# Kernel tuning notes

Hardware: AMD Instinct MI355X
Metric: run time of the kernel (lower is better)

Reference implementation:

```python
import jax, jax.numpy as jnp
import numpy as np

M, T, D, H = 2, 2048, 1024, 16
HD = D // H
SCALE = 1.0 / np.sqrt(D).astype(np.float32)  # original divides by sqrt(emb_dim)


def setup_inputs() -> dict:
    key = jax.random.key(0)
    ks = jax.random.split(key, 8)
    def lin(k):
        kw, kb = jax.random.split(k)
        W = jax.random.normal(kw, (D, D), dtype=jnp.float32) * (1.0 / np.sqrt(D))
        b = jax.random.normal(kb, (D,), dtype=jnp.float32) * 0.01
        return W, b
    Wq, bq = lin(ks[0]); Wk, bk = lin(ks[1]); Wv, bv = lin(ks[2]); Wo, bo = lin(ks[3])
    Q = jax.random.normal(ks[4], (M, T, D), dtype=jnp.float32)
    K = jax.random.normal(ks[5], (M, T, D), dtype=jnp.float32)
    V = jax.random.normal(ks[6], (M, T, D), dtype=jnp.float32)
    mask = jnp.ones((M, 1, 1, T), dtype=jnp.int32)
    return {"Q": Q, "K": K, "V": V, "mask": mask,
            "Wq": Wq, "bq": bq, "Wk": Wk, "bk": bk,
            "Wv": Wv, "bv": bv, "Wo": Wo, "bo": bo}


def reference(Q, K, V, mask, Wq, bq, Wk, bk, Wv, bv, Wo, bo):
    m = Q.shape[0]
    # torch nn.Linear: y = x @ W.T + b
    q = (Q @ Wq.T + bq).reshape(m, -1, H, HD)  # (m, Tq, h, hd)
    k = (K @ Wk.T + bk).reshape(m, -1, H, HD)
    v = (V @ Wv.T + bv).reshape(m, -1, H, HD)
    energy = jnp.einsum('mqhd,mkhd->mhqk', q, k) * SCALE
    if mask is not None:
        energy = jnp.where(mask == 0, jnp.float32(-1e20), energy)
    attn = jax.nn.softmax(energy, axis=3)  # dropout is identity at inference
    out = jnp.einsum('mhqk,mkhd->mqhd', attn, v)  # (m, Tq, h, hd)
    concat = out.reshape(m, -1, H * HD)
    return concat @ Wo.T + bo
```

## Files before the change

kernel.cpp:

```cpp
#include <hip/hip_runtime.h>
#include <cstdint>
#include <cstddef>

#define T_SEQ 2048
#define D_EMB 1024
#define H_HEADS 16
#define MROWS 4096
#define SC2 (0.03125f * 1.44269504f)
#define MASKNEG (-1e30f)

typedef __attribute__((ext_vector_type(8))) short bf16x8;
typedef __attribute__((ext_vector_type(4))) float f32x4;
typedef __attribute__((ext_vector_type(4))) unsigned short us4;

__device__ __forceinline__ unsigned short f2bf(float f) {
  union { float f; uint32_t u; } v; v.f = f;
  uint32_t u = v.u;
  return (unsigned short)((u + 0x7FFFu + ((u >> 16) & 1u)) >> 16);
}

__device__ __forceinline__ uint32_t cvtpk(float lo, float hi) {
  uint32_t r;
  asm("v_cvt_pk_bf16_f32 %0, %1, %2" : "=v"(r) : "v"(lo), "v"(hi));
  return r;
}

__device__ __forceinline__ float fexp2(float x) {
  float r;
  asm("v_exp_f32 %0, %1" : "=v"(r) : "v"(x));
  return r;
}

__device__ __forceinline__ void gl16(const void* g, void* l) {
  __builtin_amdgcn_global_load_lds(
      (const __attribute__((address_space(1))) unsigned int*)g,
      (__attribute__((address_space(3))) unsigned int*)l, 16, 0, 0);
}

__global__ __launch_bounds__(256) void cvt_all(
    const float* __restrict__ Q, const float* __restrict__ K, const float* __restrict__ V,
    const float* __restrict__ Wq, const float* __restrict__ Wk,
    const float* __restrict__ Wv, const float* __restrict__ Wo,
    unsigned short* __restrict__ Qb, unsigned short* __restrict__ Kb,
    unsigned short* __restrict__ Vb,
    unsigned short* __restrict__ Wqb, unsigned short* __restrict__ Wkb,
    unsigned short* __restrict__ Wvb, unsigned short* __restrict__ Wob) {
  int i = blockIdx.x * 256 + threadIdx.x;
  const float* src;
  unsigned short* dst;
  int j;
  if (i < 3145728) {
    int s = i >> 20;
    j = i & 1048575;
    src = (s == 0) ? Q : (s == 1) ? K : V;
    dst = (s == 0) ? Qb : (s == 1) ? Kb : Vb;
  } else {
    int k = i - 3145728;
    int s = k >> 18;
    j = k & 262143;
    src = (s == 0) ? Wq : (s == 1) ? Wk : (s == 2) ? Wv : Wo;
    dst = (s == 0) ? Wqb : (s == 1) ? Wkb : (s == 2) ? Wvb : Wob;
  }
  float4 f = ((const float4*)src)[j];
  us4 o;
  o[0] = f2bf(f.x); o[1] = f2bf(f.y); o[2] = f2bf(f.z); o[3] = f2bf(f.w);
  ((us4*)dst)[j] = o;
}

__global__ __launch_bounds__(256) void qkv_gemm(
    const unsigned short* __restrict__ Qb, const unsigned short* __restrict__ Kb,
    const unsigned short* __restrict__ Vb,
    const unsigned short* __restrict__ Wqb, const unsigned short* __restrict__ Wkb,
    const unsigned short* __restrict__ Wvb,
    const float* __restrict__ bq, const float* __restrict__ bk, const float* __restrict__ bv,
    unsigned short* __restrict__ qo, unsigned short* __restrict__ ko,
    unsigned short* __restrict__ vto) {
  const int swz = (blockIdx.x & 7) * 96 + (blockIdx.x >> 3);
  const int bx = swz & 7, by = (swz >> 3) & 31, z = swz >> 8;
  const unsigned short* A = (z == 0) ? Qb : (z == 1) ? Kb : Vb;
  const unsigned short* W = (z == 0) ? Wqb : (z == 1) ? Wkb : Wvb;
  const float* bias = (z == 0) ? bq : (z == 1) ? bk : bv;

  __shared__ __align__(16) unsigned short Asm[2][128 * 32];
  __shared__ __align__(16) unsigned short Bsm[2][128 * 32];

  const int tid = threadIdx.x;
  const int lane = tid & 63, w = tid >> 6;
  const int fq = lane >> 4, fr = lane & 15;
  const int brow = by * 128, bcol = bx * 128;
  const int wr = (w >> 1) * 64, wc = (w & 1) * 64;

  f32x4 acc[4][4] = {};

#define QKV_STAGE(buf, k0)                                                     \
  {                                                                            \
    _Pragma("unroll") for (int it = 0; it < 2; ++it) {                         \
      int idx = it * 256 + tid;                                                \
      int row = idx >> 2, ce = (idx & 3) * 8;                                  \
      gl16(&A[(size_t)(brow + row) * D_EMB + (k0) + ce],                       \
           (char*)Asm[buf] + idx * 16);                                        \
      gl16(&W[(size_t)(bcol + row) * D_EMB + (k0) + ce],                       \
           (char*)Bsm[buf] + idx * 16);                                        \
    }                                                                          \
  }

#define QKV_COMPUTE(buf)                                                       \
  {                                                                            \
    bf16x8 af[4], bfr[4];                                                      \
    _Pragma("unroll") for (int i = 0; i < 4; ++i)                              \
        af[i] = *(const bf16x8*)((const char*)Asm[buf] +                       \
                                 (wr + i * 16 + fr) * 64 + fq * 16);           \
    _Pragma("unroll") for (int j = 0; j < 4; ++j)                              \
        bfr[j] = *(const bf16x8*)((const char*)Bsm[buf] +                      \
                                  (wc + j * 16 + fr) * 64 + fq * 16);          \
    _Pragma("unroll") for (int i = 0; i < 4; ++i)                              \
        _Pragma("unroll") for (int j = 0; j < 4; ++j)                          \
            acc[i][j] = __builtin_amdgcn_mfma_f32_16x16x32_bf16(               \
                af[i], bfr[j], acc[i][j], 0, 0, 0);                            \
  }

  QKV_STAGE(0, 0);
  __syncthreads();
#pragma unroll 1
  for (int t = 0; t < 32; t += 2) {
    QKV_STAGE(1, (t + 1) * 32);
    QKV_COMPUTE(0);
    __syncthreads();
    if (t + 2 < 32) QKV_STAGE(0, (t + 2) * 32);
    QKV_COMPUTE(1);
    __syncthreads();
  }

#pragma unroll
  for (int i = 0; i < 4; ++i) {
#pragma unroll
    for (int j = 0; j < 4; ++j) {
      int r0 = brow + wr + i * 16 + fq * 4;
      int cc = bcol + wc + j * 16 + fr;
      float bb = bias[cc];
      if (z < 2) {
        unsigned short* O = (z == 0) ? qo : ko;
#pragma unroll
        for (int q = 0; q < 4; ++q)
          O[(size_t)(r0 + q) * D_EMB + cc] = f2bf(acc[i][j][q] + bb);
      } else {
        int hh = cc >> 6, dd = cc & 63;
        int mm = r0 >> 11, tt = r0 & 2047;
        us4 pk;
#pragma unroll
        for (int q = 0; q < 4; ++q) pk[q] = f2bf(acc[i][j][q] + bb);
        *(us4*)&vto[((size_t)((mm * H_HEADS + hh) * 64 + dd)) * T_SEQ + tt] = pk;
      }
    }
  }
}

__global__ __launch_bounds__(256) void out_gemm(const unsigned short* __restrict__ Ab,
                                                const unsigned short* __restrict__ Wb,
                                                const float* __restrict__ bias,
                                                float* __restrict__ Out) {
  const int swz = (blockIdx.x & 7) * 64 + (blockIdx.x >> 3);
  const int bx = swz & 15, by = swz >> 4;

  __shared__ __align__(16) unsigned short Asm[2][128 * 32];
  __shared__ __align__(16) unsigned short Bsm[2][64 * 32];
  const int tid = threadIdx.x;
  const int lane = tid & 63, w = tid >> 6;
  const int fq = lane >> 4, fr = lane & 15;
  const int brow = by * 128, bcol = bx * 64;
  const int wr = w * 32;

  f32x4 acc[2][4] = {};

#define OUT_STAGE(buf, k0)                                                     \
  {                                                                            \
    _Pragma("unroll") for (int it = 0; it < 2; ++it) {                         \
      int idx = it * 256 + tid;                                                \
      int row = idx >> 2, ce = (idx & 3) * 8;                                  \
      gl16(&Ab[(size_t)(brow + row) * D_EMB + (k0) + ce],                      \
           (char*)Asm[buf] + idx * 16);                                        \
    }                                                                          \
    {                                                                          \
      int row = tid >> 2, ce = (tid & 3) * 8;                                  \
      gl16(&Wb[(size_t)(bcol + row) * D_EMB + (k0) + ce],                      \
           (char*)Bsm[buf] + tid * 16);                                        \
    }                                                                          \
  }

#define OUT_COMPUTE(buf)                                                       \
  {                                                                            \
    bf16x8 af[2], bfr[4];                                                      \
    _Pragma("unroll") for (int i = 0; i < 2; ++i)                              \
        af[i] = *(const bf16x8*)((const char*)Asm[buf] +                       \
                                 (wr + i * 16 + fr) * 64 + fq * 16);           \
    _Pragma("unroll") for (int j = 0; j < 4; ++j)                              \
        bfr[j] = *(const bf16x8*)((const char*)Bsm[buf] +                      \
                                  (j * 16 + fr) * 64 + fq * 16);               \
    _Pragma("unroll") for (int i = 0; i < 2; ++i)                              \
        _Pragma("unroll") for (int j = 0; j < 4; ++j)                          \
            acc[i][j] = __builtin_amdgcn_mfma_f32_16x16x32_bf16(               \
                af[i], bfr[j], acc[i][j], 0, 0, 0);                            \
  }

  OUT_STAGE(0, 0);
  __syncthreads();
#pragma unroll 1
  for (int t = 0; t < 32; t += 2) {
    OUT_STAGE(1, (t + 1) * 32);
    OUT_COMPUTE(0);
    __syncthreads();
    if (t + 2 < 32) OUT_STAGE(0, (t + 2) * 32);
    OUT_COMPUTE(1);
    __syncthreads();
  }

#pragma unroll
  for (int i = 0; i < 2; ++i)
#pragma unroll
    for (int j = 0; j < 4; ++j) {
      int r0 = brow + wr + i * 16 + fq * 4;
      int cc = bcol + j * 16 + fr;
      float bb = bias[cc];
#pragma unroll
      for (int q = 0; q < 4; ++q)
        Out[(size_t)(r0 + q) * D_EMB + cc] = acc[i][j][q] + bb;
    }
}

__global__ __launch_bounds__(256) void attn_fwd(const unsigned short* __restrict__ qb,
                                                const unsigned short* __restrict__ kb,
                                                const unsigned short* __restrict__ vtb,
                                                const int* __restrict__ maskg,
                                                unsigned short* __restrict__ outb) {
  const int swzb = (blockIdx.x & 7) * 128 + (blockIdx.x >> 3);
  const int qt = swzb & 31, h = (swzb >> 5) & 15, mI = swzb >> 9;
  const int tid = threadIdx.x;
  const int lane = tid & 63, w = tid >> 6;
  const int fq = lane >> 4, fr = lane & 15;
  const int x_fr = (fr & 7) << 4;

  __shared__ __align__(16) unsigned short Ksm[128 * 64];
  __shared__ __align__(16) unsigned short Vsm[64 * 128];
  __shared__ __align__(16) unsigned short Psm[4][16 * 128];
  __shared__ __align__(16) float Msm[128];

  char* KsmB = (char*)Ksm;
  char* VsmB = (char*)Vsm;
  char* PsmB = (char*)Psm + w * 4096;

  const int qrow = qt * 64 + w * 16 + fr;
  bf16x8 qf[2];
#pragma unroll
  for (int kk = 0; kk < 2; ++kk)
    qf[kk] = *(const bf16x8*)&qb[((size_t)(mI * T_SEQ) + qrow) * D_EMB + h * 64 + kk * 32 + fq * 8];

  f32x4 o[4] = {};
  float mi = -1e30f, li = 0.f;

  const unsigned short* kpan = kb + (size_t)(mI * T_SEQ) * D_EMB + h * 64;
  const unsigned short* vpan = vtb + (size_t)(mI * H_HEADS + h) * 64 * T_SEQ;

  for (int k0 = 0; k0 < T_SEQ; k0 += 128) {
#pragma unroll
    for (int it = 0; it < 4; ++it) {
      int idx = it * 256 + tid;
      int row = idx >> 3;
      int sb = ((idx & 7) * 16) ^ ((row & 7) << 4);
      gl16(kpan + (size_t)(k0 + row) * D_EMB + (sb >> 1), KsmB + idx * 16);
    }
#pragma unroll
    for (int it = 0; it < 4; ++it) {
      int idx = it * 256 + tid;
      int row = idx >> 4;
      int sb = ((idx & 15) * 16) ^ ((row & 7) << 4);
      gl16(vpan + (size_t)row * T_SEQ + k0 + (sb >> 1), VsmB + idx * 16);
    }
    if (tid < 128) Msm[tid] = (maskg[mI * T_SEQ + k0 + tid] == 0) ? MASKNEG : 0.f;
    __syncthreads();

    f32x4 s[8];
#pragma unroll
    for (int mt = 0; mt < 8; ++mt) {
      const char* kr = KsmB + (mt * 16 + fr) * 128;
      bf16x8 a0 = *(const bf16x8*)(kr + ((fq * 16) ^ x_fr));
      bf16x8 a1 = *(const bf16x8*)(kr + ((64 + fq * 16) ^ x_fr));
      f32x4 t = {};
      t = __builtin_amdgcn_mfma_f32_16x16x32_bf16(a0, qf[0], t, 0, 0, 0);
      t = __builtin_amdgcn_mfma_f32_16x16x32_bf16(a1, qf[1], t, 0, 0, 0);
      s[mt] = t;
    }

    float tmax = -3e38f;
#pragma unroll
    for (int mt = 0; mt < 8; ++mt) {
      f32x4 mk = *(const f32x4*)&Msm[mt * 16 + fq * 4];
#pragma unroll
      for (int j = 0; j < 4; ++j) {
        float sv = fmaf(s[mt][j], SC2, mk[j]);
        s[mt][j] = sv;
        tmax = fmaxf(tmax, sv);
      }
    }
    tmax = fmaxf(tmax, __shfl_xor(tmax, 16));
    tmax = fmaxf(tmax, __shfl_xor(tmax, 32));

    if (__any(tmax > mi + 8.f)) {
      float mnew = fmaxf(mi, tmax);
      float corr = fexp2(mi - mnew);
#pragma unroll
      for (int nt = 0; nt < 4; ++nt) {
        o[nt][0] *= corr; o[nt][1] *= corr; o[nt][2] *= corr; o[nt][3] *= corr;
      }
      li *= corr;
      mi = mnew;
    }

    float ts = 0.f;
#pragma unroll
    for (int mt = 0; mt < 8; ++mt)
#pragma unroll
      for (int j = 0; j < 4; ++j) {
        float p = fexp2(s[mt][j] - mi);
        s[mt][j] = p;
        ts += p;
      }
    ts += __shfl_xor(ts, 16);
    ts += __shfl_xor(ts, 32);
    li += ts;

#pragma unroll
    for (int mt = 0; mt < 8; ++mt) {
      uint2 pw;
      pw.x = cvtpk(s[mt][0], s[mt][1]);
      pw.y = cvtpk(s[mt][2], s[mt][3]);
      *(uint2*)(PsmB + fr * 256 + ((mt * 32 + fq * 8) ^ x_fr)) = pw;
    }

    bf16x8 pb[4];
#pragma unroll
    for (int kk = 0; kk < 4; ++kk)
      pb[kk] = *(const bf16x8*)(PsmB + fr * 256 + ((kk * 64 + fq * 16) ^ x_fr));
#pragma unroll
    for (int nt = 0; nt < 4; ++nt) {
      const char* vr = VsmB + (nt * 16 + fr) * 256;
#pragma unroll
      for (int kk = 0; kk < 4; ++kk) {
        bf16x8 va = *(const bf16x8*)(vr + ((kk * 64 + fq * 16) ^ x_fr));
        o[nt] = __builtin_amdgcn_mfma_f32_16x16x32_bf16(va, pb[kk], o[nt], 0, 0, 0);
      }
    }
    __syncthreads();
  }

  float inv = 1.f / li;
  size_t orow = (size_t)(mI * T_SEQ + qt * 64 + w * 16 + fr) * D_EMB + h * 64;
#pragma unroll
  for (int nt = 0; nt < 4; ++nt) {
    uint2 ow;
    ow.x = cvtpk(o[nt][0] * inv, o[nt][1] * inv);
    ow.y = cvtpk(o[nt][2] * inv, o[nt][3] * inv);
    *(uint2*)&outb[orow + nt * 16 + fq * 4] = ow;
  }
}

extern "C" void kernel_launch(void* const* d_in, const int* in_sizes, int n_in,
                              void* d_out, int out_size, void* d_ws, size_t ws_size,
                              hipStream_t stream) {
  const float* Q  = (const float*)d_in[0];
  const float* K  = (const float*)d_in[1];
  const float* V  = (const float*)d_in[2];
  const int* mask = (const int*)d_in[3];
  const float* Wq = (const float*)d_in[4];
  const float* bq = (const float*)d_in[5];
  const float* Wk = (const float*)d_in[6];
  const float* bk = (const float*)d_in[7];
  const float* Wv = (const float*)d_in[8];
  const float* bv = (const float*)d_in[9];
  const float* Wo = (const float*)d_in[10];
  const float* bo = (const float*)d_in[11];

  uint8_t* ws = (uint8_t*)d_ws;
  const size_t MB = 1u << 20;
  unsigned short* Wq_b = (unsigned short*)(ws + 0 * MB);
  unsigned short* Wk_b = (unsigned short*)(ws + 2 * MB);
  unsigned short* Wv_b = (unsigned short*)(ws + 4 * MB);
  unsigned short* Wo_b = (unsigned short*)(ws + 6 * MB);
  unsigned short* q_b  = (unsigned short*)(ws + 8 * MB);
  unsigned short* k_b  = (unsigned short*)(ws + 16 * MB);
  unsigned short* vt_b = (unsigned short*)(ws + 24 * MB);
  unsigned short* Qb   = (unsigned short*)(ws + 32 * MB);
  unsigned short* Kb   = (unsigned short*)(ws + 40 * MB);
  unsigned short* Vb   = (unsigned short*)(ws + 48 * MB);
  unsigned short* cc_b = (unsigned short*)(ws + 32 * MB);

  cvt_all<<<dim3(16384), dim3(256), 0, stream>>>(Q, K, V, Wq, Wk, Wv, Wo,
                                                 Qb, Kb, Vb, Wq_b, Wk_b, Wv_b, Wo_b);

  qkv_gemm<<<dim3(768), dim3(256), 0, stream>>>(
      Qb, Kb, Vb, Wq_b, Wk_b, Wv_b, bq, bk, bv, q_b, k_b, vt_b);

  attn_fwd<<<dim3(1024), dim3(256), 0, stream>>>(
      q_b, k_b, vt_b, mask, cc_b);

  out_gemm<<<dim3(512), dim3(256), 0, stream>>>(
      cc_b, Wo_b, bo, (float*)d_out);
}
```

Before: 149.4 us.

## Use 32x32 MFMA attention with 128-row query tiles and folded softmax scale

The attention kernel is restructured to process 128 query rows per block (32 per wave) using 32x32x16 bf16 MFMA for both QK^T and PV, halving the grid and doubling K/V reuse per shared-memory load. The softmax scale is folded into the q projection epilogue, and a per-block mask precheck skips mask loading and addition for fully-unmasked key tiles. This reduces K/V global traffic and per-element softmax work, at the cost of more registers per wave and fewer blocks for occupancy.

```diff
diff --git a/kernel.cpp b/kernel.cpp
--- a/kernel.cpp
+++ b/kernel.cpp
@@ -11,6 +11,7 @@
 
 typedef __attribute__((ext_vector_type(8))) short bf16x8;
 typedef __attribute__((ext_vector_type(4))) float f32x4;
+typedef __attribute__((ext_vector_type(16))) float f32x16;
 typedef __attribute__((ext_vector_type(4))) unsigned short us4;
 
 __device__ __forceinline__ unsigned short f2bf(float f) {
@@ -140,9 +141,10 @@
       float bb = bias[cc];
       if (z < 2) {
         unsigned short* O = (z == 0) ? qo : ko;
+        float sc = (z == 0) ? SC2 : 1.0f;
 #pragma unroll
         for (int q = 0; q < 4; ++q)
-          O[(size_t)(r0 + q) * D_EMB + cc] = f2bf(acc[i][j][q] + bb);
+          O[(size_t)(r0 + q) * D_EMB + cc] = f2bf((acc[i][j][q] + bb) * sc);
       } else {
         int hh = cc >> 6, dd = cc & 63;
         int mm = r0 >> 11, tt = r0 & 2047;
@@ -232,35 +234,52 @@
                                                 const unsigned short* __restrict__ vtb,
                                                 const int* __restrict__ maskg,
                                                 unsigned short* __restrict__ outb) {
-  const int swzb = (blockIdx.x & 7) * 128 + (blockIdx.x >> 3);
-  const int qt = swzb & 31, h = (swzb >> 5) & 15, mI = swzb >> 9;
+  const int swzb = (blockIdx.x & 7) * 64 + (blockIdx.x >> 3);
+  const int qt = swzb & 15, h = (swzb >> 4) & 15, mI = swzb >> 8;
   const int tid = threadIdx.x;
   const int lane = tid & 63, w = tid >> 6;
-  const int fq = lane >> 4, fr = lane & 15;
-  const int x_fr = (fr & 7) << 4;
+  const int lq = lane & 31, h2 = lane >> 5;
 
   __shared__ __align__(16) unsigned short Ksm[128 * 64];
   __shared__ __align__(16) unsigned short Vsm[64 * 128];
-  __shared__ __align__(16) unsigned short Psm[4][16 * 128];
+  __shared__ __align__(16) char Pw[4][2304];
   __shared__ __align__(16) float Msm[128];
+  __shared__ int moks[16];
 
   char* KsmB = (char*)Ksm;
   char* VsmB = (char*)Vsm;
-  char* PsmB = (char*)Psm + w * 4096;
-
-  const int qrow = qt * 64 + w * 16 + fr;
-  bf16x8 qf[2];
-#pragma unroll
-  for (int kk = 0; kk < 2; ++kk)
-    qf[kk] = *(const bf16x8*)&qb[((size_t)(mI * T_SEQ) + qrow) * D_EMB + h * 64 + kk * 32 + fq * 8];
-
-  f32x4 o[4] = {};
+  char* PwB = Pw[w];
+
+  if (tid < 16) moks[tid] = 1;
+  __syncthreads();
+  {
+    int bad = 0;
+    const int4* mg = (const int4*)&maskg[mI * T_SEQ + tid * 8];
+    int4 a = mg[0], b = mg[1];
+    bad |= (a.x == 0) | (a.y == 0) | (a.z == 0) | (a.w == 0);
+    bad |= (b.x == 0) | (b.y == 0) | (b.z == 0) | (b.w == 0);
+    if (bad) moks[tid >> 4] = 0;
+  }
+  __syncthreads();
+  int okbits = 0;
+#pragma unroll
+  for (int i = 0; i < 16; ++i) okbits |= (moks[i] != 0) << i;
+
+  const int qrow = qt * 128 + w * 32 + lq;
+  bf16x8 qf[4];
+#pragma unroll
+  for (int db = 0; db < 4; ++db)
+    qf[db] = *(const bf16x8*)&qb[((size_t)(mI * T_SEQ) + qrow) * D_EMB + h * 64 + db * 16 + h2 * 8];
+
+  f32x16 oacc[2] = {};
   float mi = -1e30f, li = 0.f;
 
   const unsigned short* kpan = kb + (size_t)(mI * T_SEQ) * D_EMB + h * 64;
   const unsigned short* vpan = vtb + (size_t)(mI * H_HEADS + h) * 64 * T_SEQ;
 
+#pragma unroll 1
   for (int k0 = 0; k0 < T_SEQ; k0 += 128) {
+    const int ok = (okbits >> (k0 >> 7)) & 1;
 #pragma unroll
     for (int it = 0; it < 4; ++it) {
       int idx = it * 256 + tid;
@@ -275,92 +294,91 @@
       int sb = ((idx & 15) * 16) ^ ((row & 7) << 4);
       gl16(vpan + (size_t)row * T_SEQ + k0 + (sb >> 1), VsmB + idx * 16);
     }
-    if (tid < 128) Msm[tid] = (maskg[mI * T_SEQ + k0 + tid] == 0) ? MASKNEG : 0.f;
-    __syncthreads();
-
-    f32x4 s[8];
-#pragma unroll
-    for (int mt = 0; mt < 8; ++mt) {
-      const char* kr = KsmB + (mt * 16 + fr) * 128;
-      bf16x8 a0 = *(const bf16x8*)(kr + ((fq * 16) ^ x_fr));
-      bf16x8 a1 = *(const bf16x8*)(kr + ((64 + fq * 16) ^ x_fr));
-      f32x4 t = {};
-      t = __builtin_amdgcn_mfma_f32_16x16x32_bf16(a0, qf[0], t, 0, 0, 0);
-      t = __builtin_amdgcn_mfma_f32_16x16x32_bf16(a1, qf[1], t, 0, 0, 0);
-      s[mt] = t;
-    }
-
-    float tmax = -3e38f;
-#pragma unroll
-    for (int mt = 0; mt < 8; ++mt) {
-      f32x4 mk = *(const f32x4*)&Msm[mt * 16 + fq * 4];
-#pragma unroll
-      for (int j = 0; j < 4; ++j) {
-        float sv = fmaf(s[mt][j], SC2, mk[j]);
-        s[mt][j] = sv;
-        tmax = fmaxf(tmax, sv);
-      }
-    }
-    tmax = fmaxf(tmax, __shfl_xor(tmax, 16));
-    tmax = fmaxf(tmax, __shfl_xor(tmax, 32));
-
-    if (__any(tmax > mi + 8.f)) {
-      float mnew = fmaxf(mi, tmax);
-      float corr = fexp2(mi - mnew);
-#pragma unroll
-      for (int nt = 0; nt < 4; ++nt) {
-        o[nt][0] *= corr; o[nt][1] *= corr; o[nt][2] *= corr; o[nt][3] *= corr;
-      }
-      li *= corr;
-      mi = mnew;
-    }
-
-    float ts = 0.f;
-#pragma unroll
-    for (int mt = 0; mt < 8; ++mt)
-#pragma unroll
-      for (int j = 0; j < 4; ++j) {
-        float p = fexp2(s[mt][j] - mi);
-        s[mt][j] = p;
-        ts += p;
-      }
-    ts += __shfl_xor(ts, 16);
-    ts += __shfl_xor(ts, 32);
-    li += ts;
-
-#pragma unroll
-    for (int mt = 0; mt < 8; ++mt) {
-      uint2 pw;
-      pw.x = cvtpk(s[mt][0], s[mt][1]);
-      pw.y = cvtpk(s[mt][2], s[mt][3]);
-      *(uint2*)(PsmB + fr * 256 + ((mt * 32 + fq * 8) ^ x_fr)) = pw;
-    }
-
-    bf16x8 pb[4];
-#pragma unroll
-    for (int kk = 0; kk < 4; ++kk)
-      pb[kk] = *(const bf16x8*)(PsmB + fr * 256 + ((kk * 64 + fq * 16) ^ x_fr));
-#pragma unroll
-    for (int nt = 0; nt < 4; ++nt) {
-      const char* vr = VsmB + (nt * 16 + fr) * 256;
-#pragma unroll
-      for (int kk = 0; kk < 4; ++kk) {
-        bf16x8 va = *(const bf16x8*)(vr + ((kk * 64 + fq * 16) ^ x_fr));
-        o[nt] = __builtin_amdgcn_mfma_f32_16x16x32_bf16(va, pb[kk], o[nt], 0, 0, 0);
+    if (!ok && tid < 128) Msm[tid] = (maskg[mI * T_SEQ + k0 + tid] == 0) ? MASKNEG : 0.f;
+    __syncthreads();
+
+#pragma unroll 1
+    for (int kbk = 0; kbk < 4; ++kbk) {
+      f32x16 sv = {};
+      const int krow = kbk * 32 + lq;
+      const int kx = (krow & 7) << 4;
+#pragma unroll
+      for (int db = 0; db < 4; ++db) {
+        bf16x8 kf = *(const bf16x8*)(KsmB + krow * 128 + ((db * 32 + h2 * 16) ^ kx));
+        sv = __builtin_amdgcn_mfma_f32_32x32x16_bf16(kf, qf[db], sv, 0, 0, 0);
+      }
+      if (!ok) {
+#pragma unroll
+        for (int rg = 0; rg < 4; ++rg) {
+          f32x4 mk = *(const f32x4*)&Msm[kbk * 32 + rg * 8 + h2 * 4];
+          sv[rg * 4 + 0] += mk[0]; sv[rg * 4 + 1] += mk[1];
+          sv[rg * 4 + 2] += mk[2]; sv[rg * 4 + 3] += mk[3];
+        }
+      }
+      float a0 = fmaxf(fmaxf(sv[0], sv[1]), fmaxf(sv[2], sv[3]));
+      float a1 = fmaxf(fmaxf(sv[4], sv[5]), fmaxf(sv[6], sv[7]));
+      float a2 = fmaxf(fmaxf(sv[8], sv[9]), fmaxf(sv[10], sv[11]));
+      float a3 = fmaxf(fmaxf(sv[12], sv[13]), fmaxf(sv[14], sv[15]));
+      float tm = fmaxf(fmaxf(a0, a1), fmaxf(a2, a3));
+      tm = fmaxf(tm, __shfl_xor(tm, 32));
+      if (__any(tm > mi + 8.f)) {
+        float mnew = fmaxf(mi, tm);
+        float corr = fexp2(mi - mnew);
+#pragma unroll
+        for (int r = 0; r < 16; ++r) { oacc[0][r] *= corr; oacc[1][r] *= corr; }
+        li *= corr;
+        mi = mnew;
+      }
+#pragma unroll
+      for (int r = 0; r < 16; ++r) sv[r] = fexp2(sv[r] - mi);
+      float s0 = (sv[0] + sv[1]) + (sv[2] + sv[3]);
+      float s1 = (sv[4] + sv[5]) + (sv[6] + sv[7]);
+      float s2 = (sv[8] + sv[9]) + (sv[10] + sv[11]);
+      float s3 = (sv[12] + sv[13]) + (sv[14] + sv[15]);
+      float ts = (s0 + s1) + (s2 + s3);
+      ts += __shfl_xor(ts, 32);
+      li += ts;
+#pragma unroll
+      for (int rg = 0; rg < 4; ++rg) {
+        uint2 pw;
+        pw.x = cvtpk(sv[rg * 4 + 0], sv[rg * 4 + 1]);
+        pw.y = cvtpk(sv[rg * 4 + 2], sv[rg * 4 + 3]);
+        *(uint2*)(PwB + lq * 72 + rg * 16 + h2 * 8) = pw;
+      }
+      bf16x8 pf[2];
+#pragma unroll
+      for (int sb2 = 0; sb2 < 2; ++sb2) {
+        union { bf16x8 v; uint2 d[2]; } u;
+        u.d[0] = *(const uint2*)(PwB + lq * 72 + sb2 * 32 + h2 * 16);
+        u.d[1] = *(const uint2*)(PwB + lq * 72 + sb2 * 32 + h2 * 16 + 8);
+        pf[sb2] = u.v;
+      }
+      const int vx = (lq & 7) << 4;
+#pragma unroll
+      for (int vb = 0; vb < 2; ++vb) {
+        const int vrow = vb * 32 + lq;
+        const char* vbase = VsmB + vrow * 256;
+#pragma unroll
+        for (int sb2 = 0; sb2 < 2; ++sb2) {
+          bf16x8 vf = *(const bf16x8*)(vbase + ((kbk * 64 + sb2 * 32 + h2 * 16) ^ vx));
+          oacc[vb] = __builtin_amdgcn_mfma_f32_32x32x16_bf16(vf, pf[sb2], oacc[vb], 0, 0, 0);
+        }
       }
     }
     __syncthreads();
   }
 
   float inv = 1.f / li;
-  size_t orow = (size_t)(mI * T_SEQ + qt * 64 + w * 16 + fr) * D_EMB + h * 64;
-#pragma unroll
-  for (int nt = 0; nt < 4; ++nt) {
-    uint2 ow;
-    ow.x = cvtpk(o[nt][0] * inv, o[nt][1] * inv);
-    ow.y = cvtpk(o[nt][2] * inv, o[nt][3] * inv);
-    *(uint2*)&outb[orow + nt * 16 + fq * 4] = ow;
-  }
+  size_t orow = (size_t)(mI * T_SEQ + qrow) * D_EMB + h * 64;
+#pragma unroll
+  for (int vb = 0; vb < 2; ++vb)
+#pragma unroll
+    for (int rg = 0; rg < 4; ++rg) {
+      uint2 ow;
+      ow.x = cvtpk(oacc[vb][rg * 4 + 0] * inv, oacc[vb][rg * 4 + 1] * inv);
+      ow.y = cvtpk(oacc[vb][rg * 4 + 2] * inv, oacc[vb][rg * 4 + 3] * inv);
+      *(uint2*)&outb[orow + vb * 32 + rg * 8 + h2 * 4] = ow;
+    }
 }
 
 extern "C" void kernel_launch(void* const* d_in, const int* in_sizes, int n_in,
@@ -399,7 +417,7 @@
   qkv_gemm<<<dim3(768), dim3(256), 0, stream>>>(
       Qb, Kb, Vb, Wq_b, Wk_b, Wv_b, bq, bk, bv, q_b, k_b, vt_b);
 
-  attn_fwd<<<dim3(1024), dim3(256), 0, stream>>>(
+  attn_fwd<<<dim3(512), dim3(256), 0, stream>>>(
       q_b, k_b, vt_b, mask, cc_b);
 
   out_gemm<<<dim3(512), dim3(256), 0, stream>>>(
```

Result: slower. 156.4 us (+4.7%).
